# Performance work log

Measured on AMD Instinct MI355X. Metric: run time of the kernel, lower is better.

Reference implementation:

```python
import jax, jax.numpy as jnp
import numpy as np

B, S, HID = 4, 2048, 1024
NH, L, A = 8, 64, 64           # num_heads, linear_dim, attention_dim
NB = 128                        # time buckets
THETA = 10000.0


def _ln(x, g, b, eps=1e-5):
    m = x.mean(-1, keepdims=True)
    v = ((x - m) ** 2).mean(-1, keepdims=True)
    return (x - m) / jnp.sqrt(v + eps) * g + b


def _ln_na(x, eps=1e-5):  # F.layer_norm without affine
    m = x.mean(-1, keepdims=True)
    v = ((x - m) ** 2).mean(-1, keepdims=True)
    return (x - m) / jnp.sqrt(v + eps)


def _rope(x):
    # x: [B,H,S,A], full-dim interleaved RoPE (rope_partial_dim=0)
    inv = 1.0 / (THETA ** (jnp.arange(0, A, 2, dtype=jnp.float32) / A))
    f = jnp.arange(S, dtype=jnp.float32)[:, None] * inv[None, :]  # [S, A/2]
    cos, sin = jnp.cos(f), jnp.sin(f)
    e, o = x[..., ::2], x[..., 1::2]
    oe = e * cos - o * sin
    oo = o * cos + e * sin
    return jnp.stack([oe, oo], axis=-1).reshape(x.shape)


def setup_inputs() -> dict:
    key = jax.random.key(0)
    ks = jax.random.split(key, 12)
    x = jax.random.normal(ks[0], (B, S, HID), jnp.float32)
    interval = jnp.sort(jax.random.randint(ks[1], (B, S), 0, 1000000), axis=1).astype(jnp.int32)
    attn_mask = jnp.broadcast_to(jnp.tril(jnp.ones((S, S), bool)), (B, S, S))
    next_action_type = jax.random.randint(ks[2], (B, S), 0, 3).astype(jnp.int32)
    next_mask = jax.random.randint(ks[3], (B, S), 0, 2).astype(jnp.int32)
    uvqk = 0.02 * jax.random.normal(ks[4], (HID, 2 * L * NH + 2 * A * NH), jnp.float32)
    o_w = 0.02 * jax.random.normal(ks[5], (L * NH, HID), jnp.float32)
    pos_w = 0.02 * jax.random.normal(ks[6], (2 * S - 1,), jnp.float32)
    ts_w = 0.02 * jax.random.normal(ks[7], (NB + 1,), jnp.float32)
    act_tab = (0.02 * jax.random.normal(ks[8], (4, 32), jnp.float32)).at[0].set(0.0)
    film_w = 0.02 * jax.random.normal(ks[9], (32, 2 * HID), jnp.float32)
    return {
        'x': x, 'interval': interval, 'attn_mask': attn_mask,
        'next_action_type': next_action_type, 'next_mask': next_mask,
        'ln_g': jnp.ones(HID), 'ln_b': jnp.zeros(HID),
        'uvqk': uvqk, 'o_w': o_w, 'o_b': jnp.zeros(HID),
        'pos_w': pos_w, 'ts_w': ts_w, 'act_tab': act_tab,
        'film_ln_g': jnp.ones(32), 'film_ln_b': jnp.zeros(32),
        'film_w': film_w, 'film_b': jnp.zeros(2 * HID),
        'pr_ln_g': jnp.ones(HID), 'pr_ln_b': jnp.zeros(HID),
        'r_scale': jnp.float32(0.1), 'b_scale': jnp.float32(0.1),
    }


def reference(x, interval, attn_mask, next_action_type, next_mask,
              ln_g, ln_b, uvqk, o_w, o_b, pos_w, ts_w, act_tab,
              film_ln_g, film_ln_b, film_w, film_b, pr_ln_g, pr_ln_b,
              r_scale, b_scale):
    h = _ln(x, ln_g, ln_b)
    proj = jax.nn.silu(jnp.einsum('bsh,hd->bsd', h, uvqk))
    U = proj[..., :L * NH]
    V = proj[..., L * NH:2 * L * NH]
    Q = proj[..., 2 * L * NH:2 * L * NH + A * NH]
    K = proj[..., 2 * L * NH + A * NH:]
    U = U.reshape(B, S, NH, L).transpose(0, 2, 1, 3)
    V = V.reshape(B, S, NH, L).transpose(0, 2, 1, 3)
    Q = _rope(Q.reshape(B, S, NH, A).transpose(0, 2, 1, 3))
    K = _rope(K.reshape(B, S, NH, A).transpose(0, 2, 1, 3))
    scores = jnp.einsum('bhsa,bhta->bhst', Q, K)  # [B,H,S,S]
    # bucketized time-interval bias (indices are constants, .detach in torch)
    ts = interval.astype(jnp.float32)
    ext = jnp.concatenate([ts, ts[:, S - 1:S]], axis=1)  # [B, S+1]
    diff = ext[:, 1:, None] - ext[:, None, :-1]          # [B, S, S]
    bucket = jnp.clip((jnp.log(jnp.clip(jnp.abs(diff), 1.0, None)) / 0.301).astype(jnp.int32), 0, NB)
    scores = scores + ts_w[bucket][:, None]
    # relative position bias: bias[i,j] = pos_w[S-1 + j - i]
    rel_idx = jnp.arange(S)[None, :] - jnp.arange(S)[:, None] + (S - 1)
    scores = scores + pos_w[rel_idx][None, None]
    scores = jax.nn.silu(scores) / S
    scores = jnp.where(attn_mask[:, None], scores, 0.0)
    out = _ln_na(jnp.einsum('bhst,bhtl->bhsl', scores, V))
    u_dot = (U * out).transpose(0, 2, 1, 3).reshape(B, S, NH * L)
    outputs = x + u_dot @ o_w + o_b
    # PinRec FiLM gating
    ids = (next_action_type + 1) * (next_mask == 1)
    ae = act_tab[ids]                                    # [B,S,32]
    rb = _ln(ae, film_ln_g, film_ln_b) @ film_w + film_b
    r, b = rb[..., :HID], rb[..., HID:]
    outputs = outputs + _ln(outputs, pr_ln_g, pr_ln_b) * jnp.tanh(r) * r_scale + b * b_scale
    return outputs
```

## Files before the change

kernel.cpp:

```cpp
#include <hip/hip_runtime.h>
#include <hip/hip_bf16.h>
#include <stdint.h>

#define B_    4
#define S_    2048
#define HID_  1024
#define NH_   8
#define L_    64
#define A_    64
#define NB_   128

using bf16 = __hip_bfloat16;
typedef __bf16 bf16x8 __attribute__((ext_vector_type(8)));
typedef float  f32x4  __attribute__((ext_vector_type(4)));

__device__ __forceinline__ float bf2f(bf16 v){ return __bfloat162float(v); }
__device__ __forceinline__ bf16  f2bf(float v){ return __float2bfloat16(v); }

__device__ __forceinline__ f32x4 mfma16(bf16x8 a, bf16x8 b, f32x4 c){
  return __builtin_amdgcn_mfma_f32_16x16x32_bf16(a, b, c, 0, 0, 0);
}

__device__ __forceinline__ void gll16(const void* g, void* l){
  __builtin_amdgcn_global_load_lds(
      (const __attribute__((address_space(1))) unsigned int*)g,
      (__attribute__((address_space(3))) unsigned int*)l, 16, 0, 0);
}

__global__ __launch_bounds__(256) void k_tcast(const float* __restrict__ src,
                                               bf16* __restrict__ dst, int R, int C){
  __shared__ float t[32][33];
  int c0 = blockIdx.x*32, r0 = blockIdx.y*32;
  int tx = threadIdx.x & 31, ty = threadIdx.x >> 5;
#pragma unroll
  for (int j=0;j<4;j++) t[ty+j*8][tx] = src[(size_t)(r0+ty+j*8)*C + c0+tx];
  __syncthreads();
#pragma unroll
  for (int j=0;j<4;j++) dst[(size_t)(c0+ty+j*8)*R + r0+tx] = f2bf(t[tx][ty+j*8]);
}

__global__ void k_rb4(const float* __restrict__ act_tab, const float* __restrict__ fg,
                      const float* __restrict__ fb, const float* __restrict__ fw,
                      const float* __restrict__ fbias, float* __restrict__ rb4){
  __shared__ float lnae[4][32];
  __shared__ float mv[4][2];
  int tid = threadIdx.x;
  if (tid < 128) lnae[tid>>5][tid&31] = act_tab[tid];
  __syncthreads();
  if (tid < 4){
    float s=0.f, q=0.f;
#pragma unroll
    for (int i=0;i<32;i++){ float a=lnae[tid][i]; s+=a; q+=a*a; }
    float mean = s*(1.f/32.f);
    mv[tid][0] = mean;
    mv[tid][1] = rsqrtf(q*(1.f/32.f) - mean*mean + 1e-5f);
  }
  __syncthreads();
  if (tid < 128){
    int id=tid>>5, i=tid&31;
    lnae[id][i] = (lnae[id][i]-mv[id][0])*mv[id][1]*fg[i] + fb[i];
  }
  __syncthreads();
  for (int idx=tid; idx<4*2048; idx+=256){
    int id = idx>>11, j = idx&2047;
    float acc = fbias[j];
#pragma unroll
    for (int i=0;i<32;i++) acc += lnae[id][i]*fw[i*2048+j];
    rb4[idx] = acc;
  }
}

__global__ __launch_bounds__(256) void k_ln_x(const float* __restrict__ x,
      const float* __restrict__ g, const float* __restrict__ bta, bf16* __restrict__ h){
  int row = blockIdx.x; int tid = threadIdx.x;
  const float* xr = x + (size_t)row*HID_;
  float v[4]; float sum=0.f, sq=0.f;
#pragma unroll
  for (int i=0;i<4;i++){ v[i]=xr[tid + i*256]; sum+=v[i]; sq+=v[i]*v[i]; }
#pragma unroll
  for (int o=1;o<64;o<<=1){ sum+=__shfl_xor(sum,o,64); sq+=__shfl_xor(sq,o,64); }
  __shared__ float red[2][4];
  int wid=tid>>6, lane=tid&63;
  if(lane==0){ red[0][wid]=sum; red[1][wid]=sq; }
  __syncthreads();
  sum = red[0][0]+red[0][1]+red[0][2]+red[0][3];
  sq  = red[1][0]+red[1][1]+red[1][2]+red[1][3];
  float mean = sum*(1.f/HID_);
  float rstd = rsqrtf(sq*(1.f/HID_)-mean*mean + 1e-5f);
#pragma unroll
  for (int i=0;i<4;i++){
    int c = tid+i*256;
    h[(size_t)row*HID_ + c] = f2bf((v[i]-mean)*rstd*g[c] + bta[c]);
  }
}

__global__ __launch_bounds__(256) void k_gemm_uvqk(const bf16* __restrict__ hb,
        const bf16* __restrict__ wT, bf16* __restrict__ proj){
  __shared__ __align__(16) ushort shA[128*32];
  __shared__ __align__(16) ushort shB[128*32];
  const int K = 1024;
  int bx = blockIdx.x;
  int tm = bx & 63, tn = bx >> 6;
  int brow = tm*128, bcol = tn*128;
  int tid = threadIdx.x;
  int wid = tid>>6, lane = tid&63, lr = lane&15, lg = lane>>4;
  int wm = wid>>1, wn = wid&1;
  f32x4 acc[4][4] = {};
  for (int k0=0; k0<K; k0+=32){
    __syncthreads();
#pragma unroll
    for (int i=0;i<2;i++){
      int c = tid + i*256;
      int row = c>>2, kp = (c&3)*8;
      gll16(&hb[(size_t)(brow+row)*K + k0+kp], &shA[c*8]);
      gll16(&wT[(size_t)(bcol+row)*K + k0+kp], &shB[c*8]);
    }
    __syncthreads();
    bf16x8 a[4], b[4];
#pragma unroll
    for (int m=0;m<4;m++) a[m] = *(const bf16x8*)&shA[(wm*64+m*16+lr)*32 + lg*8];
#pragma unroll
    for (int n=0;n<4;n++) b[n] = *(const bf16x8*)&shB[(wn*64+n*16+lr)*32 + lg*8];
#pragma unroll
    for (int m=0;m<4;m++)
#pragma unroll
      for (int n=0;n<4;n++)
        acc[m][n] = mfma16(a[m], b[n], acc[m][n]);
  }
#pragma unroll
  for (int m=0;m<4;m++)
#pragma unroll
    for (int n=0;n<4;n++)
#pragma unroll
      for (int r=0;r<4;r++){
        int row = brow + wm*64+m*16+lg*4+r;
        int col = bcol + wn*64+n*16+lr;
        float v = acc[m][n][r];
        proj[(size_t)row*2048 + col] = f2bf(v / (1.f + __expf(-v)));
      }
}

__global__ __launch_bounds__(256) void k_rope(bf16* __restrict__ proj){
  int row = blockIdx.x;
  int s = row & (S_-1);
  int t = threadIdx.x;
  int h = t >> 5, p = t & 31;
  const float L2_10000 = 13.287712379549449f;
  float inv = exp2f(-(float)p * (L2_10000/32.f));
  float f = (float)s * inv;
  float sn, c; sincosf(f, &sn, &c);
  size_t base = (size_t)row*2048;
  int cq = 1024 + h*64 + 2*p;
  float qe = bf2f(proj[base+cq]), qo = bf2f(proj[base+cq+1]);
  proj[base+cq]   = f2bf(qe*c - qo*sn);
  proj[base+cq+1] = f2bf(qo*c + qe*sn);
  int ck = 1536 + h*64 + 2*p;
  float ke = bf2f(proj[base+ck]), ko = bf2f(proj[base+ck+1]);
  proj[base+ck]   = f2bf(ke*c - ko*sn);
  proj[base+ck+1] = f2bf(ko*c + ke*sn);
}

__global__ __launch_bounds__(256) void k_vtrans(const bf16* __restrict__ proj, bf16* __restrict__ Vt){
  __shared__ __align__(16) ushort lds[32][520];
  int bx = blockIdx.x; int b = bx>>6; int s0 = (bx&63)*32;
  int tid = threadIdx.x;
#pragma unroll
  for (int i=0;i<8;i++){
    int c = tid + i*256;
    int sl = c>>6, e8 = (c&63)*8;
    *(uint4*)&lds[sl][e8] = *(const uint4*)&proj[((size_t)(b*S_+s0+sl))*2048 + 512 + e8];
  }
  __syncthreads();
#pragma unroll
  for (int q=0;q<2;q++){
    int hl = tid + q*256;
    ushort v[32];
#pragma unroll
    for (int j=0;j<32;j++) v[j] = lds[j][hl];
#pragma unroll
    for (int w=0;w<4;w++)
      *(uint4*)&Vt[((size_t)b*512 + hl)*S_ + s0 + w*8] = *(uint4*)&v[w*8];
  }
}

__global__ __launch_bounds__(256, 4) void k_attn(const bf16* __restrict__ proj,
     const bf16* __restrict__ Vt, const int* __restrict__ interval,
     const float* __restrict__ ts_w, const float* __restrict__ pos_w,
     bf16* __restrict__ u_dot){
  __shared__ __align__(16) bf16 Plds[4][32][36];
  __shared__ float redbuf[4][16][65];
  int bx = blockIdx.x;
  int st = bx >> 5;
  int b  = (bx >> 3) & 3;
  int h  = bx & 7;
  int s0 = st*32;
  int tid = threadIdx.x, wid = tid>>6, lane = tid&63, lr = lane&15, lg = lane>>4;
  size_t rowb = (size_t)b * S_;
  const int* itv = interval + b*S_;

  bf16x8 aq[2][2];
#pragma unroll
  for (int m=0;m<2;m++)
#pragma unroll
    for (int ks=0;ks<2;ks++)
      aq[m][ks] = *(const bf16x8*)&proj[(rowb + s0 + m*16 + lr)*2048 + 1024 + h*64 + ks*32 + lg*8];

  int iv1[2][4];
#pragma unroll
  for (int m=0;m<2;m++)
#pragma unroll
    for (int r=0;r<4;r++){
      int sg = s0 + m*16 + lg*4 + r;
      int sp = sg+1; if (sp > S_-1) sp = S_-1;
      iv1[m][r] = itv[sp];
    }

  f32x4 acc[2][4] = {};
  int nT = st + 1;
  for (int tt = wid; tt < nT; tt += 4){
    int t0 = tt*32;
    bf16x8 kb[2][2];
#pragma unroll
    for (int n=0;n<2;n++)
#pragma unroll
      for (int ks=0;ks<2;ks++)
        kb[n][ks] = *(const bf16x8*)&proj[(rowb + t0 + n*16 + lr)*2048 + 1536 + h*64 + ks*32 + lg*8];
    f32x4 sacc[2][2] = {};
#pragma unroll
    for (int m=0;m<2;m++)
#pragma unroll
      for (int n=0;n<2;n++)
#pragma unroll
        for (int ks=0;ks<2;ks++)
          sacc[m][n] = mfma16(aq[m][ks], kb[n][ks], sacc[m][n]);
#pragma unroll
    for (int n=0;n<2;n++){
      int tg = t0 + n*16 + lr;
      int i0 = itv[tg];
#pragma unroll
      for (int m=0;m<2;m++)
#pragma unroll
        for (int r=0;r<4;r++){
          int sl = m*16 + lg*4 + r;
          int sg = s0 + sl;
          float d = fabsf((float)(iv1[m][r] - i0));
          d = fmaxf(d, 1.f);
          int bkt = (int)(__log2f(d) * 2.3027481f);
          bkt = bkt < 0 ? 0 : (bkt > NB_ ? NB_ : bkt);
          float v = sacc[m][n][r] + ts_w[bkt] + pos_w[tg - sg + (S_-1)];
          float p = v * __builtin_amdgcn_rcpf(1.f + __expf(-v)) * (1.f/(float)S_);
          Plds[wid][sl][n*16+lr] = f2bf(tg <= sg ? p : 0.f);
        }
    }
    bf16x8 pa[2];
#pragma unroll
    for (int m=0;m<2;m++) pa[m] = *(const bf16x8*)&Plds[wid][m*16+lr][lg*8];
    bf16x8 bv[4];
#pragma unroll
    for (int n=0;n<4;n++)
      bv[n] = *(const bf16x8*)&Vt[((size_t)b*512 + h*64 + n*16+lr)*S_ + t0 + lg*8];
#pragma unroll
    for (int m=0;m<2;m++)
#pragma unroll
      for (int n=0;n<4;n++)
        acc[m][n] = mfma16(pa[m], bv[n], acc[m][n]);
  }

#pragma unroll
  for (int m=0;m<2;m++){
    __syncthreads();
#pragma unroll
    for (int n=0;n<4;n++)
#pragma unroll
      for (int r=0;r<4;r++)
        redbuf[wid][lg*4+r][n*16+lr] = acc[m][n][r];
    __syncthreads();
#pragma unroll
    for (int q=0;q<4;q++){
      int rr = wid*4 + q;
      float v = redbuf[0][rr][lane] + redbuf[1][rr][lane]
              + redbuf[2][rr][lane] + redbuf[3][rr][lane];
      float sum = v, sq = v*v;
#pragma unroll
      for (int o=1;o<64;o<<=1){ sum += __shfl_xor(sum,o,64); sq += __shfl_xor(sq,o,64); }
      float mean = sum*(1.f/64.f);
      float rstd = rsqrtf(sq*(1.f/64.f) - mean*mean + 1e-5f);
      int sg = s0 + m*16 + rr;
      float u = bf2f(proj[(rowb+sg)*2048 + h*64 + lane]);
      u_dot[(rowb+sg)*512 + h*64 + lane] = f2bf((v-mean)*rstd*u);
    }
  }
}

__global__ __launch_bounds__(256) void k_gemm_out(const bf16* __restrict__ ud,
        const bf16* __restrict__ wT, const float* __restrict__ x,
        const float* __restrict__ ob, float* __restrict__ out){
  __shared__ __align__(16) ushort shA[128*32];
  __shared__ __align__(16) ushort shB[128*32];
  const int K = 512;
  int bx = blockIdx.x;
  int tm = bx & 63, tn = bx >> 6;
  int brow = tm*128, bcol = tn*128;
  int tid = threadIdx.x;
  int wid = tid>>6, lane = tid&63, lr = lane&15, lg = lane>>4;
  int wm = wid>>1, wn = wid&1;
  f32x4 acc[4][4] = {};
  for (int k0=0; k0<K; k0+=32){
    __syncthreads();
#pragma unroll
    for (int i=0;i<2;i++){
      int c = tid + i*256;
      int row = c>>2, kp = (c&3)*8;
      gll16(&ud[(size_t)(brow+row)*K + k0+kp], &shA[c*8]);
      gll16(&wT[(size_t)(bcol+row)*K + k0+kp], &shB[c*8]);
    }
    __syncthreads();
    bf16x8 a[4], b[4];
#pragma unroll
    for (int m=0;m<4;m++) a[m] = *(const bf16x8*)&shA[(wm*64+m*16+lr)*32 + lg*8];
#pragma unroll
    for (int n=0;n<4;n++) b[n] = *(const bf16x8*)&shB[(wn*64+n*16+lr)*32 + lg*8];
#pragma unroll
    for (int m=0;m<4;m++)
#pragma unroll
      for (int n=0;n<4;n++)
        acc[m][n] = mfma16(a[m], b[n], acc[m][n]);
  }
#pragma unroll
  for (int m=0;m<4;m++)
#pragma unroll
    for (int n=0;n<4;n++)
#pragma unroll
      for (int r=0;r<4;r++){
        int row = brow + wm*64+m*16+lg*4+r;
        int col = bcol + wn*64+n*16+lr;
        out[(size_t)row*HID_ + col] = acc[m][n][r] + x[(size_t)row*HID_ + col] + ob[col];
      }
}

__global__ __launch_bounds__(256) void k_film(float* __restrict__ out,
   const float* __restrict__ rb4, const int* __restrict__ nat, const int* __restrict__ nm,
   const float* __restrict__ prg, const float* __restrict__ prb,
   const float* __restrict__ rsp, const float* __restrict__ bsp){
  int row = blockIdx.x; int tid = threadIdx.x;
  float* orow = out + (size_t)row*HID_;
  int id = (nat[row] + 1) * (nm[row]==1 ? 1 : 0);
  float rs = rsp[0], bs = bsp[0];
  float v[4]; float sum=0.f, sq=0.f;
#pragma unroll
  for (int i=0;i<4;i++){ v[i]=orow[tid+i*256]; sum+=v[i]; sq+=v[i]*v[i]; }
#pragma unroll
  for (int o=1;o<64;o<<=1){ sum+=__shfl_xor(sum,o,64); sq+=__shfl_xor(sq,o,64); }
  __shared__ float red[2][4];
  int wid=tid>>6, lane=tid&63;
  if(lane==0){ red[0][wid]=sum; red[1][wid]=sq; }
  __syncthreads();
  sum = red[0][0]+red[0][1]+red[0][2]+red[0][3];
  sq  = red[1][0]+red[1][1]+red[1][2]+red[1][3];
  float mean = sum*(1.f/HID_);
  float rstd = rsqrtf(sq*(1.f/HID_)-mean*mean + 1e-5f);
#pragma unroll
  for (int i=0;i<4;i++){
    int c = tid+i*256;
    float ln = (v[i]-mean)*rstd*prg[c]+prb[c];
    float r  = rb4[id*2048 + c];
    float b2 = rb4[id*2048 + 1024 + c];
    orow[c] = v[i] + ln*tanhf(r)*rs + b2*bs;
  }
}

extern "C" void kernel_launch(void* const* d_in, const int* in_sizes, int n_in,
                              void* d_out, int out_size, void* d_ws, size_t ws_size,
                              hipStream_t stream){
  const float* x        = (const float*)d_in[0];
  const int*   interval = (const int*)d_in[1];
  const int*   nat      = (const int*)d_in[3];
  const int*   nm       = (const int*)d_in[4];
  const float* ln_g     = (const float*)d_in[5];
  const float* ln_b     = (const float*)d_in[6];
  const float* uvqk     = (const float*)d_in[7];
  const float* o_w      = (const float*)d_in[8];
  const float* o_b      = (const float*)d_in[9];
  const float* pos_w    = (const float*)d_in[10];
  const float* ts_w     = (const float*)d_in[11];
  const float* act_tab  = (const float*)d_in[12];
  const float* film_g   = (const float*)d_in[13];
  const float* film_bt  = (const float*)d_in[14];
  const float* film_w   = (const float*)d_in[15];
  const float* film_b   = (const float*)d_in[16];
  const float* pr_g     = (const float*)d_in[17];
  const float* pr_b     = (const float*)d_in[18];
  const float* r_scale  = (const float*)d_in[19];
  const float* b_scale  = (const float*)d_in[20];
  float* out = (float*)d_out;

  char* ws = (char*)d_ws;
  bf16*  uvqkT = (bf16*)(ws);
  bf16*  o_wT  = (bf16*)(ws + (4u<<20));
  float* rb4   = (float*)(ws + (5u<<20));
  bf16*  hb    = (bf16*)(ws + (6u<<20));
  bf16*  Vt    = (bf16*)(ws + (6u<<20));
  bf16*  ud    = (bf16*)(ws + (14u<<20));
  bf16*  proj  = (bf16*)(ws + (22u<<20));

  k_tcast<<<dim3(2048/32, 1024/32), 256, 0, stream>>>(uvqk, uvqkT, 1024, 2048);
  k_tcast<<<dim3(1024/32,  512/32), 256, 0, stream>>>(o_w,  o_wT,   512, 1024);
  k_rb4<<<1, 256, 0, stream>>>(act_tab, film_g, film_bt, film_w, film_b, rb4);
  k_ln_x<<<B_*S_, 256, 0, stream>>>(x, ln_g, ln_b, hb);
  k_gemm_uvqk<<<64*16, 256, 0, stream>>>(hb, uvqkT, proj);
  k_rope<<<B_*S_, 256, 0, stream>>>(proj);
  k_vtrans<<<B_*64, 256, 0, stream>>>(proj, Vt);
  k_attn<<<64*32, 256, 0, stream>>>(proj, Vt, interval, ts_w, pos_w, ud);
  k_gemm_out<<<64*8, 256, 0, stream>>>(ud, o_wT, x, o_b, out);
  k_film<<<B_*S_, 256, 0, stream>>>(out, rb4, nat, nm, pr_g, pr_b, r_scale, b_scale);
}
```

Baseline: 236.3 us.

## Restructure attention: heads per wave, paired causal row tiles, shared bias in LDS

The attention kernel now launches 256 blocks of 512 threads. Each of the 8 waves handles one head, and each block processes a pair of 16-row query tiles taken from opposite ends of the sequence so the causal work per block is balanced. The interval/position/time-bucket bias is computed once per tile into double-buffered LDS and shared across the 8 heads, with interval, pos_w and ts_w staged in LDS. The cross-wave LDS reduction is replaced by an in-register LayerNorm. The cost is a block-wide barrier every tile and only 256 blocks, which may underfill the GPU.

```diff
diff --git a/kernel.cpp b/kernel.cpp
--- a/kernel.cpp
+++ b/kernel.cpp
@@ -183,111 +183,132 @@
   }
 }
 
-__global__ __launch_bounds__(256, 4) void k_attn(const bf16* __restrict__ proj,
+__global__ __launch_bounds__(512, 2) void k_attn(const bf16* __restrict__ proj,
      const bf16* __restrict__ Vt, const int* __restrict__ interval,
      const float* __restrict__ ts_w, const float* __restrict__ pos_w,
      bf16* __restrict__ u_dot){
-  __shared__ __align__(16) bf16 Plds[4][32][36];
-  __shared__ float redbuf[4][16][65];
+  __shared__ int   itvL[2048];
+  __shared__ float posL[2080];
+  __shared__ float tsL[132];
+  __shared__ float biasT[2][16][33];
+  __shared__ __align__(16) bf16 Plds[8][16][36];
+
   int bx = blockIdx.x;
-  int st = bx >> 5;
-  int b  = (bx >> 3) & 3;
-  int h  = bx & 7;
-  int s0 = st*32;
+  int b = (bx & 7) >> 1;
+  int q = ((bx >> 3) << 1) | (bx & 1);
   int tid = threadIdx.x, wid = tid>>6, lane = tid&63, lr = lane&15, lg = lane>>4;
+  int h = wid;
   size_t rowb = (size_t)b * S_;
+  const int s0A = 16*q, s0B = 2032 - 16*q;
+  const int ntA = (s0A >> 5) + 1, ntB = (s0B >> 5) + 1;
+  const int pbase = 16*q;
+
   const int* itv = interval + b*S_;
-
-  bf16x8 aq[2][2];
-#pragma unroll
-  for (int m=0;m<2;m++)
-#pragma unroll
-    for (int ks=0;ks<2;ks++)
-      aq[m][ks] = *(const bf16x8*)&proj[(rowb + s0 + m*16 + lr)*2048 + 1024 + h*64 + ks*32 + lg*8];
-
-  int iv1[2][4];
-#pragma unroll
-  for (int m=0;m<2;m++)
+  for (int i = tid; i < 2048; i += 512) itvL[i] = itv[i];
+  for (int i = tid; i < 2080; i += 512) posL[i] = pos_w[pbase + i];
+  if (tid < 129) tsL[tid] = ts_w[tid];
+
+  bf16x8 aqA[2], aqB[2];
+#pragma unroll
+  for (int ks=0;ks<2;ks++){
+    aqA[ks] = *(const bf16x8*)&proj[(rowb + s0A + lr)*2048 + 1024 + h*64 + ks*32 + lg*8];
+    aqB[ks] = *(const bf16x8*)&proj[(rowb + s0B + lr)*2048 + 1024 + h*64 + ks*32 + lg*8];
+  }
+  f32x4 accA[4] = {}, accB[4] = {};
+
+  int bsl = tid >> 5, btl = tid & 31;
+
+#define BIAS_TILE(ss0, tt0, buf) {                                        \
+    int sg_ = (ss0) + bsl, tg_ = (tt0) + btl;                             \
+    int sp_ = sg_ + 1; if (sp_ > 2047) sp_ = 2047;                        \
+    int i1_ = itvL[sp_], i0_ = itvL[tg_];                                 \
+    float d_ = fmaxf(fabsf((float)(i1_ - i0_)), 1.f);                     \
+    int bk_ = (int)(__log2f(d_) * 2.3027481f);                            \
+    bk_ = bk_ < 0 ? 0 : (bk_ > NB_ ? NB_ : bk_);                          \
+    biasT[buf][bsl][btl] = tsL[bk_] + posL[tg_ - sg_ + 2047 - pbase];     \
+  }
+
+  __syncthreads();
+  BIAS_TILE(s0A, 0, 0);
+  __syncthreads();
+
+#define ATTN_STEP(AQ, ACC, SS0, T0, HASNXT, NS0, NT0, JG) {               \
+    bf16x8 kb[2][2];                                                      \
+_Pragma("unroll")                                                         \
+    for (int n=0;n<2;n++)                                                 \
+_Pragma("unroll")                                                         \
+      for (int ks=0;ks<2;ks++)                                            \
+        kb[n][ks] = *(const bf16x8*)&proj[(rowb + (T0) + n*16 + lr)*2048  \
+                          + 1536 + h*64 + ks*32 + lg*8];                  \
+    f32x4 sacc[2] = {};                                                   \
+_Pragma("unroll")                                                         \
+    for (int n=0;n<2;n++)                                                 \
+_Pragma("unroll")                                                         \
+      for (int ks=0;ks<2;ks++)                                            \
+        sacc[n] = mfma16(AQ[ks], kb[n][ks], sacc[n]);                     \
+    int buf_ = (JG) & 1;                                                  \
+_Pragma("unroll")                                                         \
+    for (int n=0;n<2;n++)                                                 \
+_Pragma("unroll")                                                         \
+      for (int r=0;r<4;r++){                                              \
+        int sl_ = lg*4 + r, tl_ = n*16 + lr;                              \
+        int sg_ = (SS0) + sl_, tg_ = (T0) + tl_;                          \
+        float v_ = sacc[n][r] + biasT[buf_][sl_][tl_];                    \
+        float p_ = v_ * __builtin_amdgcn_rcpf(1.f + __expf(-v_))          \
+                      * (1.f/(float)S_);                                  \
+        Plds[wid][sl_][tl_] = f2bf(tg_ <= sg_ ? p_ : 0.f);                \
+      }                                                                   \
+    if (HASNXT) BIAS_TILE(NS0, NT0, buf_^1);                              \
+    bf16x8 pa = *(const bf16x8*)&Plds[wid][lr][lg*8];                     \
+_Pragma("unroll")                                                         \
+    for (int n=0;n<4;n++){                                                \
+      bf16x8 bv = *(const bf16x8*)&Vt[((size_t)b*512 + h*64 + n*16+lr)*S_ \
+                                      + (T0) + lg*8];                     \
+      ACC[n] = mfma16(pa, bv, ACC[n]);                                    \
+    }                                                                     \
+    __syncthreads();                                                      \
+  }
+
+  int jg = 0;
+  for (int j = 0; j < ntA; ++j, ++jg){
+    int t0 = j*32;
+    int hasnxt = 1;
+    int ns0 = (j+1 < ntA) ? s0A : s0B;
+    int nt0 = (j+1 < ntA) ? (j+1)*32 : 0;
+    ATTN_STEP(aqA, accA, s0A, t0, hasnxt, ns0, nt0, jg);
+  }
+  for (int j = 0; j < ntB; ++j, ++jg){
+    int t0 = j*32;
+    int hasnxt = (j+1 < ntB);
+    int nt0 = (j+1)*32;
+    ATTN_STEP(aqB, accB, s0B, t0, hasnxt, s0B, nt0, jg);
+  }
+#undef ATTN_STEP
+#undef BIAS_TILE
+
+#pragma unroll
+  for (int si=0; si<2; ++si){
+    int s0 = si ? s0B : s0A;
 #pragma unroll
     for (int r=0;r<4;r++){
-      int sg = s0 + m*16 + lg*4 + r;
-      int sp = sg+1; if (sp > S_-1) sp = S_-1;
-      iv1[m][r] = itv[sp];
-    }
-
-  f32x4 acc[2][4] = {};
-  int nT = st + 1;
-  for (int tt = wid; tt < nT; tt += 4){
-    int t0 = tt*32;
-    bf16x8 kb[2][2];
-#pragma unroll
-    for (int n=0;n<2;n++)
-#pragma unroll
-      for (int ks=0;ks<2;ks++)
-        kb[n][ks] = *(const bf16x8*)&proj[(rowb + t0 + n*16 + lr)*2048 + 1536 + h*64 + ks*32 + lg*8];
-    f32x4 sacc[2][2] = {};
-#pragma unroll
-    for (int m=0;m<2;m++)
-#pragma unroll
-      for (int n=0;n<2;n++)
-#pragma unroll
-        for (int ks=0;ks<2;ks++)
-          sacc[m][n] = mfma16(aq[m][ks], kb[n][ks], sacc[m][n]);
-#pragma unroll
-    for (int n=0;n<2;n++){
-      int tg = t0 + n*16 + lr;
-      int i0 = itv[tg];
-#pragma unroll
-      for (int m=0;m<2;m++)
-#pragma unroll
-        for (int r=0;r<4;r++){
-          int sl = m*16 + lg*4 + r;
-          int sg = s0 + sl;
-          float d = fabsf((float)(iv1[m][r] - i0));
-          d = fmaxf(d, 1.f);
-          int bkt = (int)(__log2f(d) * 2.3027481f);
-          bkt = bkt < 0 ? 0 : (bkt > NB_ ? NB_ : bkt);
-          float v = sacc[m][n][r] + ts_w[bkt] + pos_w[tg - sg + (S_-1)];
-          float p = v * __builtin_amdgcn_rcpf(1.f + __expf(-v)) * (1.f/(float)S_);
-          Plds[wid][sl][n*16+lr] = f2bf(tg <= sg ? p : 0.f);
-        }
-    }
-    bf16x8 pa[2];
-#pragma unroll
-    for (int m=0;m<2;m++) pa[m] = *(const bf16x8*)&Plds[wid][m*16+lr][lg*8];
-    bf16x8 bv[4];
-#pragma unroll
-    for (int n=0;n<4;n++)
-      bv[n] = *(const bf16x8*)&Vt[((size_t)b*512 + h*64 + n*16+lr)*S_ + t0 + lg*8];
-#pragma unroll
-    for (int m=0;m<2;m++)
-#pragma unroll
-      for (int n=0;n<4;n++)
-        acc[m][n] = mfma16(pa[m], bv[n], acc[m][n]);
-  }
-
-#pragma unroll
-  for (int m=0;m<2;m++){
-    __syncthreads();
-#pragma unroll
-    for (int n=0;n<4;n++)
-#pragma unroll
-      for (int r=0;r<4;r++)
-        redbuf[wid][lg*4+r][n*16+lr] = acc[m][n][r];
-    __syncthreads();
-#pragma unroll
-    for (int q=0;q<4;q++){
-      int rr = wid*4 + q;
-      float v = redbuf[0][rr][lane] + redbuf[1][rr][lane]
-              + redbuf[2][rr][lane] + redbuf[3][rr][lane];
-      float sum = v, sq = v*v;
-#pragma unroll
-      for (int o=1;o<64;o<<=1){ sum += __shfl_xor(sum,o,64); sq += __shfl_xor(sq,o,64); }
+      float v0 = si ? accB[0][r] : accA[0][r];
+      float v1 = si ? accB[1][r] : accA[1][r];
+      float v2 = si ? accB[2][r] : accA[2][r];
+      float v3 = si ? accB[3][r] : accA[3][r];
+      float sum = v0+v1+v2+v3;
+      float sq  = v0*v0+v1*v1+v2*v2+v3*v3;
+#pragma unroll
+      for (int o=1;o<16;o<<=1){ sum += __shfl_xor(sum,o,64); sq += __shfl_xor(sq,o,64); }
       float mean = sum*(1.f/64.f);
       float rstd = rsqrtf(sq*(1.f/64.f) - mean*mean + 1e-5f);
-      int sg = s0 + m*16 + rr;
-      float u = bf2f(proj[(rowb+sg)*2048 + h*64 + lane]);
-      u_dot[(rowb+sg)*512 + h*64 + lane] = f2bf((v-mean)*rstd*u);
+      int sg = s0 + lg*4 + r;
+      float vv[4] = {v0,v1,v2,v3};
+#pragma unroll
+      for (int n=0;n<4;n++){
+        int col = n*16+lr;
+        float u = bf2f(proj[(rowb+sg)*2048 + h*64 + col]);
+        u_dot[(rowb+sg)*512 + h*64 + col] = f2bf((vv[n]-mean)*rstd*u);
+      }
     }
   }
 }
@@ -410,7 +431,7 @@
   k_gemm_uvqk<<<64*16, 256, 0, stream>>>(hb, uvqkT, proj);
   k_rope<<<B_*S_, 256, 0, stream>>>(proj);
   k_vtrans<<<B_*64, 256, 0, stream>>>(proj, Vt);
-  k_attn<<<64*32, 256, 0, stream>>>(proj, Vt, interval, ts_w, pos_w, ud);
+  k_attn<<<256, 512, 0, stream>>>(proj, Vt, interval, ts_w, pos_w, ud);
   k_gemm_out<<<64*8, 256, 0, stream>>>(ud, o_wT, x, o_b, out);
   k_film<<<B_*S_, 256, 0, stream>>>(out, rb4, nat, nm, pr_g, pr_b, r_scale, b_scale);
 }
```

After: 276.6 us. 1.17x slower.

## Precompute head-shared attention bias in MFMA fragment layout; reverse tile order

Applied to the files above, without the earlier changes.

Adds a kernel that computes the timestamp-bucket plus relative-position bias once per batch and causal tile, in bf16 and in MFMA fragment order. The attention kernel no longer recomputes it for each of the 8 heads. The causal mask is folded in as a -10000 bias so silu yields roughly zero, and the 1/S scale moves after the PV reduction. The attention grid is reordered to launch the longest row tiles first, and the occupancy hint is raised from 4 to 6. In exchange, the bias is rounded to bf16 and must be read back from global memory on every tile.

```diff
diff --git a/kernel.cpp b/kernel.cpp
--- a/kernel.cpp
+++ b/kernel.cpp
@@ -183,20 +183,63 @@
   }
 }
 
-__global__ __launch_bounds__(256, 4) void k_attn(const bf16* __restrict__ proj,
-     const bf16* __restrict__ Vt, const int* __restrict__ interval,
-     const float* __restrict__ ts_w, const float* __restrict__ pos_w,
+__global__ __launch_bounds__(256) void k_bias_sw(const int* __restrict__ interval,
+      const float* __restrict__ ts_w, const float* __restrict__ pos_w,
+      bf16* __restrict__ bsw){
+  __shared__ int   itvL[2048];
+  __shared__ float posL[2080];
+  __shared__ float tsL[132];
+  int bx = blockIdx.x;
+  int b  = bx & 3;
+  int st = 63 - (bx >> 2);
+  int tid = threadIdx.x, wid = tid>>6, lane = tid&63, lr = lane&15, lg = lane>>4;
+  const int* itv = interval + b*S_;
+  for (int i=tid;i<2048;i+=256) itvL[i]=itv[i];
+  int pbase = 2016 - st*32;
+  int plen  = st*32 + 63;
+  for (int i=tid;i<plen;i+=256) posL[i] = pos_w[pbase + i];
+  if (tid<129) tsL[tid]=ts_w[tid];
+  __syncthreads();
+  size_t tbase = (size_t)b*2080 + (size_t)(st*(st+1)/2);
+  for (int tt = wid; tt <= st; tt += 4){
+    ushort ov[16];
+#pragma unroll
+    for (int m=0;m<2;m++)
+#pragma unroll
+      for (int n=0;n<2;n++)
+#pragma unroll
+        for (int r=0;r<4;r++){
+          int sl = m*16 + lg*4 + r;
+          int sg = st*32 + sl;
+          int tg = tt*32 + n*16 + lr;
+          float val;
+          if (tg <= sg){
+            int sp = sg+1; if (sp>2047) sp=2047;
+            float d = fmaxf(fabsf((float)(itvL[sp]-itvL[tg])),1.f);
+            int bk = (int)(__log2f(d)*2.3027481f);
+            bk = bk<0?0:(bk>NB_?NB_:bk);
+            val = tsL[bk] + posL[tg - sl + 31];
+          } else val = -10000.f;
+          ov[m*8+n*4+r] = __bfloat16_as_ushort(f2bf(val));
+        }
+    bf16* dst = bsw + ((tbase + tt)*64 + lane)*16;
+    *(uint4*)dst     = *(uint4*)&ov[0];
+    *(uint4*)(dst+8) = *(uint4*)&ov[8];
+  }
+}
+
+__global__ __launch_bounds__(256, 6) void k_attn(const bf16* __restrict__ proj,
+     const bf16* __restrict__ Vt, const bf16* __restrict__ bsw,
      bf16* __restrict__ u_dot){
   __shared__ __align__(16) bf16 Plds[4][32][36];
   __shared__ float redbuf[4][16][65];
   int bx = blockIdx.x;
-  int st = bx >> 5;
+  int st = 63 - (bx >> 5);
   int b  = (bx >> 3) & 3;
   int h  = bx & 7;
   int s0 = st*32;
   int tid = threadIdx.x, wid = tid>>6, lane = tid&63, lr = lane&15, lg = lane>>4;
   size_t rowb = (size_t)b * S_;
-  const int* itv = interval + b*S_;
 
   bf16x8 aq[2][2];
 #pragma unroll
@@ -205,16 +248,7 @@
     for (int ks=0;ks<2;ks++)
       aq[m][ks] = *(const bf16x8*)&proj[(rowb + s0 + m*16 + lr)*2048 + 1024 + h*64 + ks*32 + lg*8];
 
-  int iv1[2][4];
-#pragma unroll
-  for (int m=0;m<2;m++)
-#pragma unroll
-    for (int r=0;r<4;r++){
-      int sg = s0 + m*16 + lg*4 + r;
-      int sp = sg+1; if (sp > S_-1) sp = S_-1;
-      iv1[m][r] = itv[sp];
-    }
-
+  size_t tbase = (size_t)b*2080 + (size_t)(st*(st+1)/2);
   f32x4 acc[2][4] = {};
   int nT = st + 1;
   for (int tt = wid; tt < nT; tt += 4){
@@ -225,6 +259,9 @@
 #pragma unroll
       for (int ks=0;ks<2;ks++)
         kb[n][ks] = *(const bf16x8*)&proj[(rowb + t0 + n*16 + lr)*2048 + 1536 + h*64 + ks*32 + lg*8];
+    const bf16* bp = bsw + ((tbase + tt)*64 + lane)*16;
+    bf16x8 bb0 = *(const bf16x8*)bp;
+    bf16x8 bb1 = *(const bf16x8*)(bp+8);
     f32x4 sacc[2][2] = {};
 #pragma unroll
     for (int m=0;m<2;m++)
@@ -234,36 +271,26 @@
         for (int ks=0;ks<2;ks++)
           sacc[m][n] = mfma16(aq[m][ks], kb[n][ks], sacc[m][n]);
 #pragma unroll
-    for (int n=0;n<2;n++){
-      int tg = t0 + n*16 + lr;
-      int i0 = itv[tg];
+    for (int m=0;m<2;m++)
+#pragma unroll
+      for (int n=0;n<2;n++)
+#pragma unroll
+        for (int r=0;r<4;r++){
+          float bv = bf2f(m ? (bf16)bb1[n*4+r] : (bf16)bb0[n*4+r]);
+          float v  = sacc[m][n][r] + bv;
+          float p  = v * __builtin_amdgcn_rcpf(1.f + __expf(-v));
+          Plds[wid][m*16 + lg*4 + r][n*16 + lr] = f2bf(p);
+        }
+    bf16x8 pa[2];
+#pragma unroll
+    for (int m=0;m<2;m++) pa[m] = *(const bf16x8*)&Plds[wid][m*16+lr][lg*8];
+#pragma unroll
+    for (int n=0;n<4;n++){
+      bf16x8 bv = *(const bf16x8*)&Vt[((size_t)b*512 + h*64 + n*16+lr)*S_ + t0 + lg*8];
 #pragma unroll
       for (int m=0;m<2;m++)
-#pragma unroll
-        for (int r=0;r<4;r++){
-          int sl = m*16 + lg*4 + r;
-          int sg = s0 + sl;
-          float d = fabsf((float)(iv1[m][r] - i0));
-          d = fmaxf(d, 1.f);
-          int bkt = (int)(__log2f(d) * 2.3027481f);
-          bkt = bkt < 0 ? 0 : (bkt > NB_ ? NB_ : bkt);
-          float v = sacc[m][n][r] + ts_w[bkt] + pos_w[tg - sg + (S_-1)];
-          float p = v * __builtin_amdgcn_rcpf(1.f + __expf(-v)) * (1.f/(float)S_);
-          Plds[wid][sl][n*16+lr] = f2bf(tg <= sg ? p : 0.f);
-        }
+        acc[m][n] = mfma16(pa[m], bv, acc[m][n]);
     }
-    bf16x8 pa[2];
-#pragma unroll
-    for (int m=0;m<2;m++) pa[m] = *(const bf16x8*)&Plds[wid][m*16+lr][lg*8];
-    bf16x8 bv[4];
-#pragma unroll
-    for (int n=0;n<4;n++)
-      bv[n] = *(const bf16x8*)&Vt[((size_t)b*512 + h*64 + n*16+lr)*S_ + t0 + lg*8];
-#pragma unroll
-    for (int m=0;m<2;m++)
-#pragma unroll
-      for (int n=0;n<4;n++)
-        acc[m][n] = mfma16(pa[m], bv[n], acc[m][n]);
   }
 
 #pragma unroll
@@ -278,8 +305,8 @@
 #pragma unroll
     for (int q=0;q<4;q++){
       int rr = wid*4 + q;
-      float v = redbuf[0][rr][lane] + redbuf[1][rr][lane]
-              + redbuf[2][rr][lane] + redbuf[3][rr][lane];
+      float v = (redbuf[0][rr][lane] + redbuf[1][rr][lane]
+               + redbuf[2][rr][lane] + redbuf[3][rr][lane]) * (1.f/(float)S_);
       float sum = v, sq = v*v;
 #pragma unroll
       for (int o=1;o<64;o<<=1){ sum += __shfl_xor(sum,o,64); sq += __shfl_xor(sq,o,64); }
@@ -402,15 +429,17 @@
   bf16*  Vt    = (bf16*)(ws + (6u<<20));
   bf16*  ud    = (bf16*)(ws + (14u<<20));
   bf16*  proj  = (bf16*)(ws + (22u<<20));
+  bf16*  bsw   = (bf16*)(ws + (54u<<20));
 
   k_tcast<<<dim3(2048/32, 1024/32), 256, 0, stream>>>(uvqk, uvqkT, 1024, 2048);
   k_tcast<<<dim3(1024/32,  512/32), 256, 0, stream>>>(o_w,  o_wT,   512, 1024);
   k_rb4<<<1, 256, 0, stream>>>(act_tab, film_g, film_bt, film_w, film_b, rb4);
+  k_bias_sw<<<256, 256, 0, stream>>>(interval, ts_w, pos_w, bsw);
   k_ln_x<<<B_*S_, 256, 0, stream>>>(x, ln_g, ln_b, hb);
   k_gemm_uvqk<<<64*16, 256, 0, stream>>>(hb, uvqkT, proj);
   k_rope<<<B_*S_, 256, 0, stream>>>(proj);
   k_vtrans<<<B_*64, 256, 0, stream>>>(proj, Vt);
-  k_attn<<<64*32, 256, 0, stream>>>(proj, Vt, interval, ts_w, pos_w, ud);
+  k_attn<<<64*32, 256, 0, stream>>>(proj, Vt, bsw, ud);
   k_gemm_out<<<64*8, 256, 0, stream>>>(ud, o_wT, x, o_b, out);
   k_film<<<B_*S_, 256, 0, stream>>>(out, rb4, nat, nm, pr_g, pr_b, r_scale, b_scale);
 }
```

After: 254.8 us. 1.08x slower.
